# Optimization experiments

Measured on AMD Instinct MI355X. Metric: run time of the kernel, lower is better.

## Reference

```python
import jax, jax.numpy as jnp
import numpy as np

N_PTS = 1_000_000  # number of sample points (i index)
M_COMP = 64        # number of Gaussian components (j index)
D = 2


def setup_inputs() -> dict:
    key = jax.random.key(0)
    k1, k2, k3 = jax.random.split(key, 3)
    sample = jax.random.uniform(k1, (N_PTS, D), dtype=jnp.float32)
    mu = jax.random.uniform(k2, (M_COMP, D), dtype=jnp.float32)
    # Original init is A = 15 * I; add small noise so the Cholesky-like factor is generic.
    A = 15.0 * jnp.broadcast_to(jnp.eye(D, dtype=jnp.float32), (M_COMP, D, D)) \
        + 0.5 * jax.random.normal(k3, (M_COMP, D, D), dtype=jnp.float32)
    w = jnp.ones((M_COMP, 1), dtype=jnp.float32)
    return {"sample": sample, "mu": mu, "A": A, "w": w}


def reference(sample, mu, A, w):
    """log_likelihoods(sample): log sum_j weights_j * exp(-(x_i-mu_j)^T G_j (x_i-mu_j))."""
    M = A.shape[0]
    # gamma_j = A_j A_j^T / 2  (symmetric, M x D x D)
    gamma = jnp.einsum('jkm,jlm->jkl', A, A) / 2
    g = gamma.reshape(M, D * D)  # (M, 4), row-major [g00, g01, g10, g11]
    # batched 2x2 determinant (covariances_determinants)
    dets = g[:, 0] * g[:, 3] - g[:, 1] * g[:, 2]  # (M,)
    # weights_log = log_softmax(w) + 0.5 * log(det)
    wlog = jax.nn.log_softmax(w, axis=0)[:, 0] + 0.5 * jnp.log(dets)  # (M,)
    # Weighted squared distance q_ij = (x_i - mu_j)^T G_j (x_i - mu_j),
    # expanded to avoid the (N, M, D) difference tensor:
    xx = jnp.stack([sample[:, 0] * sample[:, 0],
                    sample[:, 0] * sample[:, 1],
                    sample[:, 1] * sample[:, 0],
                    sample[:, 1] * sample[:, 1]], axis=1)  # (N, 4)
    quad_x = xx @ g.T                                      # (N, M)
    Gmu = jnp.einsum('jkl,jl->jk', gamma, mu)              # (M, D)
    cross = sample @ Gmu.T                                 # (N, M)
    const = jnp.einsum('jk,jk->j', mu, Gmu)                # (M,)
    K = -(quad_x - 2.0 * cross + const[None, :])           # (N, M) log-kernel
    # weighted logsumexp over components j
    ll = jax.nn.logsumexp(K + wlog[None, :], axis=1, keepdims=True)  # (N, 1)
    return ll
```

## Files before the change

### kernel.cpp

```cpp
#include <hip/hip_runtime.h>
#include <math.h>

#define N_PTS 1000000
#define M_COMP 64

typedef float v2f __attribute__((ext_vector_type(2)));

__device__ __forceinline__ float exp2n(float x) { return __builtin_amdgcn_exp2f(x); }
__device__ __forceinline__ float log2n(float x) { return __builtin_amdgcn_logf(x); }

__global__ __launch_bounds__(256) void gm_fused(
    const float* __restrict__ sample,
    const float* __restrict__ mu,
    const float* __restrict__ A,
    const float* __restrict__ w,
    float* __restrict__ out)
{
    __shared__ float cf[6 * M_COMP];

    const int tid = threadIdx.x;
    const float L2E = 1.4426950408889634f;
    const float LN2 = 0.6931471805599453f;

    if (tid < 64) {
        const int j = tid;
        const float a00 = A[j*4+0], a01 = A[j*4+1], a10 = A[j*4+2], a11 = A[j*4+3];
        const float g00 = 0.5f*(a00*a00 + a01*a01);
        const float g01 = 0.5f*(a00*a10 + a01*a11);
        const float g11 = 0.5f*(a10*a10 + a11*a11);
        const float det = g00*g11 - g01*g01;

        const float m0 = mu[j*2+0], m1 = mu[j*2+1];
        const float Gmu0 = g00*m0 + g01*m1;
        const float Gmu1 = g01*m0 + g11*m1;
        const float cst  = m0*Gmu0 + m1*Gmu1;

        const float wj = w[j];
        float mx = wj;
        #pragma unroll
        for (int m = 1; m < 64; m <<= 1)
            mx = fmaxf(mx, __shfl_xor(mx, m, 64));
        float se = exp2n((wj - mx) * L2E);
        #pragma unroll
        for (int m = 1; m < 64; m <<= 1)
            se += __shfl_xor(se, m, 64);
        const float lse  = mx + log2n(se) * LN2;
        const float wlog = wj - lse + 0.5f * log2n(det) * LN2;

        cf[0*M_COMP+j] = -g00 * L2E;
        cf[1*M_COMP+j] = -(g01+g01) * L2E;
        cf[2*M_COMP+j] = -g11 * L2E;
        cf[3*M_COMP+j] = (Gmu0+Gmu0) * L2E;
        cf[4*M_COMP+j] = (Gmu1+Gmu1) * L2E;
        cf[5*M_COMP+j] = (wlog - cst) * L2E;
    }
    __syncthreads();

    const int t  = blockIdx.x * 256 + tid;
    const int p0 = t * 4;
    const bool ok = p0 < N_PTS;
    const int pl = ok ? p0 : 0;

    const float4* s4 = (const float4*)sample;
    const float4 qa = s4[(pl >> 1) + 0];
    const float4 qb = s4[(pl >> 1) + 1];

    const v2f ax0 = {qa.x, qa.z}, ax1 = {qa.y, qa.w};
    const v2f bx0 = {qb.x, qb.z}, bx1 = {qb.y, qb.w};
    const v2f axx0 = ax0*ax0, ax01 = ax0*ax1, axx1 = ax1*ax1;
    const v2f bxx0 = bx0*bx0, bx01 = bx0*bx1, bxx1 = bx1*bx1;

    v2f accA = {0.f, 0.f};
    v2f accB = {0.f, 0.f};

    #pragma unroll 4
    for (int jc = 0; jc < M_COMP; jc += 4) {
        const float4 c0 = *(const float4*)&cf[0*M_COMP+jc];
        const float4 c1 = *(const float4*)&cf[1*M_COMP+jc];
        const float4 c2 = *(const float4*)&cf[2*M_COMP+jc];
        const float4 c3 = *(const float4*)&cf[3*M_COMP+jc];
        const float4 c4 = *(const float4*)&cf[4*M_COMP+jc];
        const float4 c5 = *(const float4*)&cf[5*M_COMP+jc];

#define GM_COMP(F)                                                      \
        {                                                               \
            v2f s = {c5.F, c5.F};                                       \
            s = __builtin_elementwise_fma(ax1,  (v2f){c4.F, c4.F}, s);  \
            s = __builtin_elementwise_fma(ax0,  (v2f){c3.F, c3.F}, s);  \
            s = __builtin_elementwise_fma(axx1, (v2f){c2.F, c2.F}, s);  \
            s = __builtin_elementwise_fma(ax01, (v2f){c1.F, c1.F}, s);  \
            s = __builtin_elementwise_fma(axx0, (v2f){c0.F, c0.F}, s);  \
            accA[0] += exp2n(s[0]);                                     \
            accA[1] += exp2n(s[1]);                                     \
            v2f r = {c5.F, c5.F};                                       \
            r = __builtin_elementwise_fma(bx1,  (v2f){c4.F, c4.F}, r);  \
            r = __builtin_elementwise_fma(bx0,  (v2f){c3.F, c3.F}, r);  \
            r = __builtin_elementwise_fma(bxx1, (v2f){c2.F, c2.F}, r);  \
            r = __builtin_elementwise_fma(bx01, (v2f){c1.F, c1.F}, r);  \
            r = __builtin_elementwise_fma(bxx0, (v2f){c0.F, c0.F}, r);  \
            accB[0] += exp2n(r[0]);                                     \
            accB[1] += exp2n(r[1]);                                     \
        }
        GM_COMP(x)
        GM_COMP(y)
        GM_COMP(z)
        GM_COMP(w)
#undef GM_COMP
    }

    if (ok) {
        float4 o;
        o.x = log2n(accA[0]) * LN2;
        o.y = log2n(accA[1]) * LN2;
        o.z = log2n(accB[0]) * LN2;
        o.w = log2n(accB[1]) * LN2;
        *(float4*)&out[p0] = o;
    }
}

extern "C" void kernel_launch(void* const* d_in, const int* in_sizes, int n_in,
                              void* d_out, int out_size, void* d_ws, size_t ws_size,
                              hipStream_t stream)
{
    const float* sample = (const float*)d_in[0];
    const float* mu     = (const float*)d_in[1];
    const float* A      = (const float*)d_in[2];
    const float* w      = (const float*)d_in[3];
    float* out = (float*)d_out;

    const int threads = N_PTS / 4;
    const int blocks  = (threads + 255) / 256;
    gm_fused<<<blocks, 256, 0, stream>>>(sample, mu, A, w, out);
}
```

Measured before the change: 17.80 us.

## Split coefficient setup into separate kernel and read coefficients as uniform global loads

Moves the per-component coefficient computation out of every block into a single-block precompute kernel that writes to workspace. The main kernel then reads coefficients straight from global memory with uniform indices, which the compiler can turn into scalar loads, and drops shared memory and the block barrier. This removes the redundant per-block prologue and LDS traffic at the cost of an extra kernel launch. The unroll factor also drops from 4 to 2.

```diff
diff --git a/kernel.cpp b/kernel.cpp
--- a/kernel.cpp
+++ b/kernel.cpp
@@ -9,57 +9,58 @@
 __device__ __forceinline__ float exp2n(float x) { return __builtin_amdgcn_exp2f(x); }
 __device__ __forceinline__ float log2n(float x) { return __builtin_amdgcn_logf(x); }
 
-__global__ __launch_bounds__(256) void gm_fused(
-    const float* __restrict__ sample,
+__global__ __launch_bounds__(64) void gm_coef(
     const float* __restrict__ mu,
     const float* __restrict__ A,
     const float* __restrict__ w,
-    float* __restrict__ out)
+    float* __restrict__ cf)
 {
-    __shared__ float cf[6 * M_COMP];
-
-    const int tid = threadIdx.x;
+    const int j = threadIdx.x;
     const float L2E = 1.4426950408889634f;
     const float LN2 = 0.6931471805599453f;
 
-    if (tid < 64) {
-        const int j = tid;
-        const float a00 = A[j*4+0], a01 = A[j*4+1], a10 = A[j*4+2], a11 = A[j*4+3];
-        const float g00 = 0.5f*(a00*a00 + a01*a01);
-        const float g01 = 0.5f*(a00*a10 + a01*a11);
-        const float g11 = 0.5f*(a10*a10 + a11*a11);
-        const float det = g00*g11 - g01*g01;
+    const float a00 = A[j*4+0], a01 = A[j*4+1], a10 = A[j*4+2], a11 = A[j*4+3];
+    const float g00 = 0.5f*(a00*a00 + a01*a01);
+    const float g01 = 0.5f*(a00*a10 + a01*a11);
+    const float g11 = 0.5f*(a10*a10 + a11*a11);
+    const float det = g00*g11 - g01*g01;
 
-        const float m0 = mu[j*2+0], m1 = mu[j*2+1];
-        const float Gmu0 = g00*m0 + g01*m1;
-        const float Gmu1 = g01*m0 + g11*m1;
-        const float cst  = m0*Gmu0 + m1*Gmu1;
+    const float m0 = mu[j*2+0], m1 = mu[j*2+1];
+    const float Gmu0 = g00*m0 + g01*m1;
+    const float Gmu1 = g01*m0 + g11*m1;
+    const float cst  = m0*Gmu0 + m1*Gmu1;
 
-        const float wj = w[j];
-        float mx = wj;
-        #pragma unroll
-        for (int m = 1; m < 64; m <<= 1)
-            mx = fmaxf(mx, __shfl_xor(mx, m, 64));
-        float se = exp2n((wj - mx) * L2E);
-        #pragma unroll
-        for (int m = 1; m < 64; m <<= 1)
-            se += __shfl_xor(se, m, 64);
-        const float lse  = mx + log2n(se) * LN2;
-        const float wlog = wj - lse + 0.5f * log2n(det) * LN2;
+    const float wj = w[j];
+    float mx = wj;
+    #pragma unroll
+    for (int m = 1; m < 64; m <<= 1)
+        mx = fmaxf(mx, __shfl_xor(mx, m, 64));
+    float se = exp2n((wj - mx) * L2E);
+    #pragma unroll
+    for (int m = 1; m < 64; m <<= 1)
+        se += __shfl_xor(se, m, 64);
+    const float lse  = mx + log2n(se) * LN2;
+    const float wlog = wj - lse + 0.5f * log2n(det) * LN2;
 
-        cf[0*M_COMP+j] = -g00 * L2E;
-        cf[1*M_COMP+j] = -(g01+g01) * L2E;
-        cf[2*M_COMP+j] = -g11 * L2E;
-        cf[3*M_COMP+j] = (Gmu0+Gmu0) * L2E;
-        cf[4*M_COMP+j] = (Gmu1+Gmu1) * L2E;
-        cf[5*M_COMP+j] = (wlog - cst) * L2E;
-    }
-    __syncthreads();
+    cf[0*M_COMP+j] = -g00 * L2E;
+    cf[1*M_COMP+j] = -(g01+g01) * L2E;
+    cf[2*M_COMP+j] = -g11 * L2E;
+    cf[3*M_COMP+j] = (Gmu0+Gmu0) * L2E;
+    cf[4*M_COMP+j] = (Gmu1+Gmu1) * L2E;
+    cf[5*M_COMP+j] = (wlog - cst) * L2E;
+}
 
-    const int t  = blockIdx.x * 256 + tid;
+__global__ __launch_bounds__(256) void gm_ll(
+    const float* __restrict__ sample,
+    const float* __restrict__ cf,
+    float* __restrict__ out)
+{
+    const float LN2 = 0.6931471805599453f;
+
+    const int t  = blockIdx.x * 256 + threadIdx.x;
     const int p0 = t * 4;
     const bool ok = p0 < N_PTS;
-    const int pl = ok ? p0 : 0;
+    const int  pl = ok ? p0 : 0;
 
     const float4* s4 = (const float4*)sample;
     const float4 qa = s4[(pl >> 1) + 0];
@@ -73,39 +74,35 @@
     v2f accA = {0.f, 0.f};
     v2f accB = {0.f, 0.f};
 
-    #pragma unroll 4
+    #pragma unroll 2
     for (int jc = 0; jc < M_COMP; jc += 4) {
-        const float4 c0 = *(const float4*)&cf[0*M_COMP+jc];
-        const float4 c1 = *(const float4*)&cf[1*M_COMP+jc];
-        const float4 c2 = *(const float4*)&cf[2*M_COMP+jc];
-        const float4 c3 = *(const float4*)&cf[3*M_COMP+jc];
-        const float4 c4 = *(const float4*)&cf[4*M_COMP+jc];
-        const float4 c5 = *(const float4*)&cf[5*M_COMP+jc];
+        #pragma unroll
+        for (int u = 0; u < 4; ++u) {
+            const float c0 = cf[0*M_COMP + jc + u];
+            const float c1 = cf[1*M_COMP + jc + u];
+            const float c2 = cf[2*M_COMP + jc + u];
+            const float c3 = cf[3*M_COMP + jc + u];
+            const float c4 = cf[4*M_COMP + jc + u];
+            const float c5 = cf[5*M_COMP + jc + u];
 
-#define GM_COMP(F)                                                      \
-        {                                                               \
-            v2f s = {c5.F, c5.F};                                       \
-            s = __builtin_elementwise_fma(ax1,  (v2f){c4.F, c4.F}, s);  \
-            s = __builtin_elementwise_fma(ax0,  (v2f){c3.F, c3.F}, s);  \
-            s = __builtin_elementwise_fma(axx1, (v2f){c2.F, c2.F}, s);  \
-            s = __builtin_elementwise_fma(ax01, (v2f){c1.F, c1.F}, s);  \
-            s = __builtin_elementwise_fma(axx0, (v2f){c0.F, c0.F}, s);  \
-            accA[0] += exp2n(s[0]);                                     \
-            accA[1] += exp2n(s[1]);                                     \
-            v2f r = {c5.F, c5.F};                                       \
-            r = __builtin_elementwise_fma(bx1,  (v2f){c4.F, c4.F}, r);  \
-            r = __builtin_elementwise_fma(bx0,  (v2f){c3.F, c3.F}, r);  \
-            r = __builtin_elementwise_fma(bxx1, (v2f){c2.F, c2.F}, r);  \
-            r = __builtin_elementwise_fma(bx01, (v2f){c1.F, c1.F}, r);  \
-            r = __builtin_elementwise_fma(bxx0, (v2f){c0.F, c0.F}, r);  \
-            accB[0] += exp2n(r[0]);                                     \
-            accB[1] += exp2n(r[1]);                                     \
+            v2f s = {c5, c5};
+            s = __builtin_elementwise_fma(ax1,  (v2f){c4, c4}, s);
+            s = __builtin_elementwise_fma(ax0,  (v2f){c3, c3}, s);
+            s = __builtin_elementwise_fma(axx1, (v2f){c2, c2}, s);
+            s = __builtin_elementwise_fma(ax01, (v2f){c1, c1}, s);
+            s = __builtin_elementwise_fma(axx0, (v2f){c0, c0}, s);
+            accA[0] += exp2n(s[0]);
+            accA[1] += exp2n(s[1]);
+
+            v2f r = {c5, c5};
+            r = __builtin_elementwise_fma(bx1,  (v2f){c4, c4}, r);
+            r = __builtin_elementwise_fma(bx0,  (v2f){c3, c3}, r);
+            r = __builtin_elementwise_fma(bxx1, (v2f){c2, c2}, r);
+            r = __builtin_elementwise_fma(bx01, (v2f){c1, c1}, r);
+            r = __builtin_elementwise_fma(bxx0, (v2f){c0, c0}, r);
+            accB[0] += exp2n(r[0]);
+            accB[1] += exp2n(r[1]);
         }
-        GM_COMP(x)
-        GM_COMP(y)
-        GM_COMP(z)
-        GM_COMP(w)
-#undef GM_COMP
     }
 
     if (ok) {
@@ -127,8 +124,11 @@
     const float* A      = (const float*)d_in[2];
     const float* w      = (const float*)d_in[3];
     float* out = (float*)d_out;
+    float* cf  = (float*)d_ws;
+
+    gm_coef<<<1, 64, 0, stream>>>(mu, A, w, cf);
 
     const int threads = N_PTS / 4;
     const int blocks  = (threads + 255) / 256;
-    gm_fused<<<blocks, 256, 0, stream>>>(sample, mu, A, w, out);
+    gm_ll<<<blocks, 256, 0, stream>>>(sample, cf, out);
 }
```

Result: slower. 22.04 us (+23.8%).

## Split coefficient prep into separate kernel and split components across wavefronts

Applied to the files above, without the earlier changes.

Moves the per-component coefficient computation into a tiny single-wave kernel that writes to workspace, so the main kernel no longer has every block recompute it and wait at a barrier. In the main kernel each wave of a block handles 16 of the 64 components for the same 256 points, and partial sums are combined through shared memory before the log. This gives four times more blocks and shorter per-thread loops, at the cost of an extra launch, redundant sample loads across waves, global (cached) coefficient reads instead of LDS, and a second barrier.

```diff
diff --git a/kernel.cpp b/kernel.cpp
--- a/kernel.cpp
+++ b/kernel.cpp
@@ -1,7 +1,7 @@
 #include <hip/hip_runtime.h>
 #include <math.h>
 
-#define N_PTS 1000000
+#define N_PTS  1000000
 #define M_COMP 64
 
 typedef float v2f __attribute__((ext_vector_type(2)));
@@ -9,57 +9,63 @@
 __device__ __forceinline__ float exp2n(float x) { return __builtin_amdgcn_exp2f(x); }
 __device__ __forceinline__ float log2n(float x) { return __builtin_amdgcn_logf(x); }
 
-__global__ __launch_bounds__(256) void gm_fused(
-    const float* __restrict__ sample,
+__global__ __launch_bounds__(64) void gm_coef(
     const float* __restrict__ mu,
     const float* __restrict__ A,
     const float* __restrict__ w,
-    float* __restrict__ out)
+    float* __restrict__ cf)
 {
-    __shared__ float cf[6 * M_COMP];
-
-    const int tid = threadIdx.x;
+    const int j = threadIdx.x;
     const float L2E = 1.4426950408889634f;
     const float LN2 = 0.6931471805599453f;
 
-    if (tid < 64) {
-        const int j = tid;
-        const float a00 = A[j*4+0], a01 = A[j*4+1], a10 = A[j*4+2], a11 = A[j*4+3];
-        const float g00 = 0.5f*(a00*a00 + a01*a01);
-        const float g01 = 0.5f*(a00*a10 + a01*a11);
-        const float g11 = 0.5f*(a10*a10 + a11*a11);
-        const float det = g00*g11 - g01*g01;
+    const float a00 = A[j*4+0], a01 = A[j*4+1], a10 = A[j*4+2], a11 = A[j*4+3];
+    const float g00 = 0.5f*(a00*a00 + a01*a01);
+    const float g01 = 0.5f*(a00*a10 + a01*a11);
+    const float g11 = 0.5f*(a10*a10 + a11*a11);
+    const float det = g00*g11 - g01*g01;
 
-        const float m0 = mu[j*2+0], m1 = mu[j*2+1];
-        const float Gmu0 = g00*m0 + g01*m1;
-        const float Gmu1 = g01*m0 + g11*m1;
-        const float cst  = m0*Gmu0 + m1*Gmu1;
+    const float m0 = mu[j*2+0], m1 = mu[j*2+1];
+    const float Gmu0 = g00*m0 + g01*m1;
+    const float Gmu1 = g01*m0 + g11*m1;
+    const float cst  = m0*Gmu0 + m1*Gmu1;
 
-        const float wj = w[j];
-        float mx = wj;
-        #pragma unroll
-        for (int m = 1; m < 64; m <<= 1)
-            mx = fmaxf(mx, __shfl_xor(mx, m, 64));
-        float se = exp2n((wj - mx) * L2E);
-        #pragma unroll
-        for (int m = 1; m < 64; m <<= 1)
-            se += __shfl_xor(se, m, 64);
-        const float lse  = mx + log2n(se) * LN2;
-        const float wlog = wj - lse + 0.5f * log2n(det) * LN2;
+    const float wj = w[j];
+    float mx = wj;
+    #pragma unroll
+    for (int m = 1; m < 64; m <<= 1)
+        mx = fmaxf(mx, __shfl_xor(mx, m, 64));
+    float se = exp2n((wj - mx) * L2E);
+    #pragma unroll
+    for (int m = 1; m < 64; m <<= 1)
+        se += __shfl_xor(se, m, 64);
+    const float lse  = mx + log2n(se) * LN2;
+    const float wlog = wj - lse + 0.5f * log2n(det) * LN2;
 
-        cf[0*M_COMP+j] = -g00 * L2E;
-        cf[1*M_COMP+j] = -(g01+g01) * L2E;
-        cf[2*M_COMP+j] = -g11 * L2E;
-        cf[3*M_COMP+j] = (Gmu0+Gmu0) * L2E;
-        cf[4*M_COMP+j] = (Gmu1+Gmu1) * L2E;
-        cf[5*M_COMP+j] = (wlog - cst) * L2E;
-    }
-    __syncthreads();
+    cf[0*M_COMP+j] = -g00 * L2E;
+    cf[1*M_COMP+j] = -(g01+g01) * L2E;
+    cf[2*M_COMP+j] = -g11 * L2E;
+    cf[3*M_COMP+j] = (Gmu0+Gmu0) * L2E;
+    cf[4*M_COMP+j] = (Gmu1+Gmu1) * L2E;
+    cf[5*M_COMP+j] = (wlog - cst) * L2E;
+}
 
-    const int t  = blockIdx.x * 256 + tid;
-    const int p0 = t * 4;
+__global__ __launch_bounds__(256) void gm_ll(
+    const float* __restrict__ sample,
+    const float* __restrict__ cf,
+    float* __restrict__ out)
+{
+    __shared__ float part[4][256];
+
+    const float LN2 = 0.6931471805599453f;
+    const int tid  = threadIdx.x;
+    const int L    = tid & 63;
+    const int q    = tid >> 6;
+    const int base = blockIdx.x * 256;
+
+    const int  p0 = base + 4*L;
     const bool ok = p0 < N_PTS;
-    const int pl = ok ? p0 : 0;
+    const int  pl = ok ? p0 : 0;
 
     const float4* s4 = (const float4*)sample;
     const float4 qa = s4[(pl >> 1) + 0];
@@ -73,14 +79,16 @@
     v2f accA = {0.f, 0.f};
     v2f accB = {0.f, 0.f};
 
-    #pragma unroll 4
-    for (int jc = 0; jc < M_COMP; jc += 4) {
-        const float4 c0 = *(const float4*)&cf[0*M_COMP+jc];
-        const float4 c1 = *(const float4*)&cf[1*M_COMP+jc];
-        const float4 c2 = *(const float4*)&cf[2*M_COMP+jc];
-        const float4 c3 = *(const float4*)&cf[3*M_COMP+jc];
-        const float4 c4 = *(const float4*)&cf[4*M_COMP+jc];
-        const float4 c5 = *(const float4*)&cf[5*M_COMP+jc];
+    const float* cfq = cf + q * 16;
+
+    #pragma unroll 1
+    for (int jc = 0; jc < 16; jc += 4) {
+        const float4 c0 = *(const float4*)&cfq[0*M_COMP+jc];
+        const float4 c1 = *(const float4*)&cfq[1*M_COMP+jc];
+        const float4 c2 = *(const float4*)&cfq[2*M_COMP+jc];
+        const float4 c3 = *(const float4*)&cfq[3*M_COMP+jc];
+        const float4 c4 = *(const float4*)&cfq[4*M_COMP+jc];
+        const float4 c5 = *(const float4*)&cfq[5*M_COMP+jc];
 
 #define GM_COMP(F)                                                      \
         {                                                               \
@@ -108,13 +116,16 @@
 #undef GM_COMP
     }
 
-    if (ok) {
-        float4 o;
-        o.x = log2n(accA[0]) * LN2;
-        o.y = log2n(accA[1]) * LN2;
-        o.z = log2n(accB[0]) * LN2;
-        o.w = log2n(accB[1]) * LN2;
-        *(float4*)&out[p0] = o;
+    float4 pw;
+    pw.x = accA[0]; pw.y = accA[1]; pw.z = accB[0]; pw.w = accB[1];
+    *(float4*)&part[q][4*L] = pw;
+    __syncthreads();
+
+    const int pg = base + tid;
+    if (pg < N_PTS) {
+        const float sum = part[0][tid] + part[1][tid]
+                        + part[2][tid] + part[3][tid];
+        out[pg] = log2n(sum) * LN2;
     }
 }
 
@@ -127,8 +138,10 @@
     const float* A      = (const float*)d_in[2];
     const float* w      = (const float*)d_in[3];
     float* out = (float*)d_out;
+    float* cf  = (float*)d_ws;
 
-    const int threads = N_PTS / 4;
-    const int blocks  = (threads + 255) / 256;
-    gm_fused<<<blocks, 256, 0, stream>>>(sample, mu, A, w, out);
+    gm_coef<<<1, 64, 0, stream>>>(mu, A, w, cf);
+
+    const int blocks = (N_PTS + 255) / 256;
+    gm_ll<<<blocks, 256, 0, stream>>>(sample, cf, out);
 }
```

After: 24.07 us. 35.2% more time.
